# Kernel tuning notes

Hardware: AMD Instinct MI355X
Metric: run time of the kernel (lower is better)

Reference implementation:

```python
import jax, jax.numpy as jnp
import numpy as np
from jax import lax

FEAT = 56  # features_size
SR = 2     # sr_ratio
NUM_HEADS = 8

# Constant relative-distance indices, shape (N, N, 2) with values in [0, 2*FEAT-2]
_idx = np.array([[i, j] for i in range(FEAT) for j in range(FEAT)])
REL = jnp.asarray(_idx[None, :, :] - _idx[:, None, :] + FEAT - 1)  # (N, N, 2)


def setup_inputs() -> dict:
    key = jax.random.key(0)
    ks = jax.random.split(key, 8)
    dim = 256
    B = 4
    x = jax.random.normal(ks[0], (B, dim, FEAT, FEAT), dtype=jnp.float32)
    Wq = jax.random.normal(ks[1], (dim, dim), dtype=jnp.float32) * 0.02
    Wkv = jax.random.normal(ks[2], (dim, 2 * dim), dtype=jnp.float32) * 0.02
    sr_w = jax.random.normal(ks[3], (dim, dim, SR, SR), dtype=jnp.float32) * 0.02  # OIHW
    sr_b = jnp.zeros((dim,), dtype=jnp.float32)
    ln_g = jnp.ones((dim,), dtype=jnp.float32)
    ln_b = jnp.zeros((dim,), dtype=jnp.float32)
    pos_emb = jax.random.normal(ks[4], (2 * FEAT - 1, 2 * FEAT - 1), dtype=jnp.float32) * 0.2
    proj_w = jax.random.normal(ks[5], (dim, dim), dtype=jnp.float32) * 0.02
    proj_b = jnp.zeros((dim,), dtype=jnp.float32)
    return {"x": x, "Wq": Wq, "Wkv": Wkv, "sr_w": sr_w, "sr_b": sr_b,
            "ln_g": ln_g, "ln_b": ln_b, "pos_emb": pos_emb,
            "proj_w": proj_w, "proj_b": proj_b}


def reference(x, Wq, Wkv, sr_w, sr_b, ln_g, ln_b, pos_emb, proj_w, proj_b):
    B, C, H, W = x.shape
    N = H * W
    h = NUM_HEADS
    hd = C // h
    scale = hd ** -0.5

    x_q = x.reshape(B, C, N).transpose(0, 2, 1)            # (B, N, C)
    q = (x_q @ Wq).reshape(B, N, h, hd).transpose(0, 2, 1, 3)  # (B, h, N, hd)

    # spatial reduction conv (kernel=stride=SR) + layernorm
    xr = lax.conv_general_dilated(x, sr_w, (SR, SR), 'VALID',
                                  dimension_numbers=('NCHW', 'OIHW', 'NCHW'))
    xr = xr + sr_b[None, :, None, None]
    Nk = (H // SR) * (W // SR)
    x_kv = xr.reshape(B, C, Nk).transpose(0, 2, 1)          # (B, Nk, C)
    mu = jnp.mean(x_kv, axis=-1, keepdims=True)
    var = jnp.var(x_kv, axis=-1, keepdims=True)
    x_kv = (x_kv - mu) * lax.rsqrt(var + 1e-5) * ln_g + ln_b

    # kv projection; einops '(dim h l)' split: head_dim slowest, l fastest
    kv = (x_kv @ Wkv).reshape(B, Nk, hd, h, 2)
    k = kv[..., 0].transpose(0, 3, 1, 2)                    # (B, h, Nk, hd)
    v = kv[..., 1].transpose(0, 3, 1, 2)                    # (B, h, Nk, hd)

    attn = jnp.einsum('bhnd,bhmd->bhnm', q, k) * scale      # (B, h, N, Nk)
    bias = pos_emb[REL[..., 0], REL[..., 1]][:, :Nk]        # (N, Nk)
    attn = jax.nn.softmax(attn + bias, axis=-1)

    out = jnp.einsum('bhnm,bhmd->bhnd', attn, v)            # (B, h, N, hd)
    out = out.transpose(0, 2, 1, 3).reshape(B, N, C)
    out = out @ proj_w + proj_b
    return out.transpose(0, 2, 1).reshape(B, C, H, W)
```

## Files before the change

### kernel.cpp

```cpp
#include <hip/hip_runtime.h>

typedef float f32x4 __attribute__((ext_vector_type(4)));
typedef short s16x8 __attribute__((ext_vector_type(8)));
typedef unsigned short u16x4 __attribute__((ext_vector_type(4)));

#define MFMA16(a,b,c) __builtin_amdgcn_mfma_f32_16x16x32_bf16(a,b,c,0,0,0)

#define NTOK 3136
#define NKV  784
#define NKVP 800
#define CD   256
#define NH   8
#define HD   32
#define PEW  111
#define SC2  (0.17677669529663687f * 1.4426950408889634f)

static __device__ __forceinline__ unsigned short f2b(float f){
  unsigned int u = __float_as_uint(f);
  return (unsigned short)((u + 0x7fffu + ((u>>16)&1u)) >> 16);
}
static __device__ __forceinline__ float b2f(unsigned short u){
  return __uint_as_float(((unsigned int)u)<<16);
}

__global__ void k_prepw(const float* __restrict__ Wq, const float* __restrict__ Wkv,
                        const float* __restrict__ pw, const float* __restrict__ srw,
                        unsigned short* __restrict__ WqT, unsigned short* __restrict__ WkvT,
                        unsigned short* __restrict__ pwT, unsigned short* __restrict__ srwb){
  int i = blockIdx.x*256 + threadIdx.x;
  if (i < 65536){ int nn=i>>8, kk=i&255; WqT[i] = f2b(Wq[kk*256+nn]); }
  else if (i < 196608){ int j=i-65536; int c2=j>>8, kk=j&255; WkvT[j] = f2b(Wkv[kk*512+c2]); }
  else if (i < 262144){ int j=i-196608; int cc=j>>8, kk=j&255; pwT[j] = f2b(pw[kk*256+cc]); }
  else { int j=i-262144; srwb[j] = f2b(srw[j]); }
}

__global__ void k_bias(const float* __restrict__ pos, unsigned short* __restrict__ bias2){
  int key = blockIdx.x*256 + threadIdx.x;
  int n = blockIdx.y;
  if (key >= NKVP) return;
  float v;
  if (key < NKV){
    int nr = (n*9363)>>19, nc = n - nr*56;
    int tt = (key*9363)>>19, mm = key - tt*56;
    v = pos[(tt-nr+55)*PEW + (mm-nc+55)] * 1.4426950408889634f;
  } else v = -30000.f;
  bias2[(size_t)n*NKVP + key] = f2b(v);
}

__global__ void k_pad(unsigned short* __restrict__ kb, unsigned short* __restrict__ vT){
  int i = blockIdx.x*256 + threadIdx.x;
  if (i < 16384){
    int bh=i>>9, r=i&511, key=784+(r>>5), d=r&31;
    kb[((size_t)bh*NKVP + key)*HD + d] = 0;
  } else {
    int j=i-16384;
    int bh=j>>9, r=j&511, d=r>>4, key=784+(r&15);
    vT[((size_t)bh*HD + d)*NKVP + key] = 0;
  }
}

__global__ __launch_bounds__(256) void k_qproj(const float* __restrict__ x,
      const unsigned short* __restrict__ WqT, unsigned short* __restrict__ qb){
  const int tid=threadIdx.x, wv=tid>>6, l=tid&63, g=l>>4, ln16=l&15;
  const int bI = blockIdx.x/49;
  const int n0 = (blockIdx.x%49)*64;
  const int m0 = n0 + (wv>>1)*32;
  const int c0 = blockIdx.y*64 + (wv&1)*32;
  const float* xb = x + (size_t)bI*CD*NTOK;
  f32x4 acc[2][2] = {};
  for (int k0=0; k0<CD; k0+=32){
    s16x8 a[2], bf[2];
#pragma unroll
    for (int mi=0; mi<2; ++mi){
      int n = m0 + mi*16 + ln16;
      const float* xp = xb + (size_t)(k0+g*8)*NTOK + n;
#pragma unroll
      for (int j=0;j<8;++j) a[mi][j] = (short)f2b(xp[(size_t)j*NTOK]);
    }
#pragma unroll
    for (int ni=0; ni<2; ++ni)
      bf[ni] = *(const s16x8*)&WqT[(size_t)(c0+ni*16+ln16)*CD + k0 + g*8];
#pragma unroll
    for (int mi=0;mi<2;++mi)
#pragma unroll
      for (int ni=0;ni<2;++ni) acc[mi][ni] = MFMA16(a[mi], bf[ni], acc[mi][ni]);
  }
#pragma unroll
  for (int mi=0;mi<2;++mi)
#pragma unroll
    for (int ni=0;ni<2;++ni){
      int c = c0 + ni*16 + ln16;
#pragma unroll
      for (int r=0;r<4;++r){
        int n = m0 + mi*16 + g*4 + r;
        qb[((size_t)bI*NTOK + n)*CD + c] = f2b(acc[mi][ni][r]);
      }
    }
}

__global__ __launch_bounds__(256) void k_conv(const float* __restrict__ x,
      const unsigned short* __restrict__ srwb, const float* __restrict__ srb,
      float* __restrict__ convo){
  const int tid=threadIdx.x, wv=tid>>6, l=tid&63, g=l>>4, ln16=l&15;
  const int m0 = blockIdx.x*64 + (wv>>1)*32;
  const int c0 = blockIdx.y*64 + (wv&1)*32;
  size_t abase[2];
#pragma unroll
  for (int mi=0;mi<2;++mi){
    int m = m0 + mi*16 + ln16;
    int bb = (m>=2352)?3:(m>=1568)?2:(m>=784)?1:0;
    int nk = m - bb*784;
    int pp = (nk*9363)>>18, qq = nk - pp*28;
    abase[mi] = (size_t)bb*CD*NTOK + (size_t)(2*pp)*56 + 2*qq;
  }
  const int off[8] = {0,1,56,57,3136,3137,3192,3193};
  f32x4 acc[2][2] = {};
  for (int k0=0; k0<1024; k0+=32){
    int cib = (k0>>2) + g*2;
    s16x8 a[2], bf[2];
#pragma unroll
    for (int mi=0;mi<2;++mi){
      const float* xp = x + abase[mi] + (size_t)cib*NTOK;
#pragma unroll
      for (int j=0;j<8;++j) a[mi][j] = (short)f2b(xp[off[j]]);
    }
#pragma unroll
    for (int ni=0;ni<2;++ni)
      bf[ni] = *(const s16x8*)&srwb[(size_t)(c0+ni*16+ln16)*1024 + k0 + g*8];
#pragma unroll
    for (int mi=0;mi<2;++mi)
#pragma unroll
      for (int ni=0;ni<2;++ni) acc[mi][ni] = MFMA16(a[mi], bf[ni], acc[mi][ni]);
  }
#pragma unroll
  for (int mi=0;mi<2;++mi)
#pragma unroll
    for (int ni=0;ni<2;++ni){
      int c = c0 + ni*16 + ln16;
      float bias = srb[c];
#pragma unroll
      for (int r=0;r<4;++r){
        int m = m0 + mi*16 + g*4 + r;
        convo[(size_t)m*CD + c] = acc[mi][ni][r] + bias;
      }
    }
}

__global__ void k_ln(const float* __restrict__ co, const float* __restrict__ gam,
                     const float* __restrict__ bet, unsigned short* __restrict__ kvbf){
  const int row = blockIdx.x, t = threadIdx.x;
  float v = co[(size_t)row*CD + t];
  float s = v, s2 = v*v;
#pragma unroll
  for (int o=32; o>0; o>>=1){ s += __shfl_down(s,o); s2 += __shfl_down(s2,o); }
  __shared__ float ps[4], ps2[4];
  int wid = t>>6, lane = t&63;
  if (lane==0){ ps[wid]=s; ps2[wid]=s2; }
  __syncthreads();
  if (t==0){
    float a = ps[0]+ps[1]+ps[2]+ps[3];
    float a2 = ps2[0]+ps2[1]+ps2[2]+ps2[3];
    float mu = a*(1.f/CD);
    float var = a2*(1.f/CD) - mu*mu;
    ps[0] = mu; ps2[0] = rsqrtf(var + 1e-5f);
  }
  __syncthreads();
  float mu = ps[0], rs = ps2[0];
  kvbf[(size_t)row*CD + t] = f2b((v-mu)*rs*gam[t] + bet[t]);
}

__global__ __launch_bounds__(256) void k_kv(const unsigned short* __restrict__ kvbf,
      const unsigned short* __restrict__ WkvT, unsigned short* __restrict__ kb,
      unsigned short* __restrict__ vT){
  const int tid=threadIdx.x, wv=tid>>6, l=tid&63, g=l>>4, ln16=l&15;
  const int m0 = blockIdx.x*64 + (wv>>1)*32;
  const int c0 = blockIdx.y*64 + (wv&1)*32;
  f32x4 acc[2][2] = {};
  for (int k0=0; k0<CD; k0+=32){
    s16x8 a[2], bf[2];
#pragma unroll
    for (int mi=0;mi<2;++mi)
      a[mi] = *(const s16x8*)&kvbf[(size_t)(m0+mi*16+ln16)*CD + k0 + g*8];
#pragma unroll
    for (int ni=0;ni<2;++ni)
      bf[ni] = *(const s16x8*)&WkvT[(size_t)(c0+ni*16+ln16)*CD + k0 + g*8];
#pragma unroll
    for (int mi=0;mi<2;++mi)
#pragma unroll
      for (int ni=0;ni<2;++ni) acc[mi][ni] = MFMA16(a[mi], bf[ni], acc[mi][ni]);
  }
#pragma unroll
  for (int mi=0;mi<2;++mi)
#pragma unroll
    for (int ni=0;ni<2;++ni){
      int c2 = c0 + ni*16 + ln16;
      int d = c2>>4, hh = (c2>>1)&7;
#pragma unroll
      for (int r=0;r<4;++r){
        int m = m0 + mi*16 + g*4 + r;
        int bq = (m>=2352)?3:(m>=1568)?2:(m>=784)?1:0;
        int nk = m - bq*784;
        unsigned short val = f2b(acc[mi][ni][r]);
        if (c2&1) vT[(((size_t)bq*NH+hh)*HD + d)*NKVP + nk] = val;
        else      kb[(((size_t)bq*NH+hh)*NKVP + nk)*HD + d] = val;
      }
    }
}

__global__ __launch_bounds__(256) void k_attn(const unsigned short* __restrict__ qb,
      const unsigned short* __restrict__ kb, const unsigned short* __restrict__ vT,
      const unsigned short* __restrict__ bias2, unsigned short* __restrict__ aout){
  __shared__ unsigned short Pl[4][16][40];
  const int tid=threadIdx.x, wv=tid>>6, l=tid&63, g=l>>4, ln16=l&15;
  const int bh = blockIdx.y, b = bh>>3, h = bh&7;
  const int nw = blockIdx.x*64 + wv*16;
  const s16x8 qf = *(const s16x8*)&qb[((size_t)b*NTOK + nw + ln16)*CD + h*HD + g*8];
  const unsigned short* kbp = kb + (size_t)bh*NKVP*HD;
  const unsigned short* vbp = vT + (size_t)bh*HD*NKVP;
  const unsigned short* bp  = bias2 + (size_t)(nw + ln16)*NKVP;
  f32x4 accO0 = {}, accO1 = {};
  float S = 0.f;
  const f32x4 zf = {};
  for (int ks=0; ks<NKVP; ks+=32){
    s16x8 ka0 = *(const s16x8*)&kbp[(size_t)(ks+ln16)*HD + g*8];
    s16x8 ka1 = *(const s16x8*)&kbp[(size_t)(ks+16+ln16)*HD + g*8];
    f32x4 d0 = MFMA16(ka0, qf, zf);
    f32x4 d1 = MFMA16(ka1, qf, zf);
    u16x4 bb0 = *(const u16x4*)&bp[ks + g*4];
    u16x4 bb1 = *(const u16x4*)&bp[ks + 16 + g*4];
    float p[8];
#pragma unroll
    for (int r=0;r<4;++r){
      p[r]   = exp2f(d0[r]*SC2 + b2f(bb0[r]));
      p[4+r] = exp2f(d1[r]*SC2 + b2f(bb1[r]));
    }
    S += ((p[0]+p[1])+(p[2]+p[3])) + ((p[4]+p[5])+(p[6]+p[7]));
    unsigned int w0 = (unsigned int)f2b(p[0]) | ((unsigned int)f2b(p[1])<<16);
    unsigned int w1 = (unsigned int)f2b(p[2]) | ((unsigned int)f2b(p[3])<<16);
    unsigned int w2 = (unsigned int)f2b(p[4]) | ((unsigned int)f2b(p[5])<<16);
    unsigned int w3 = (unsigned int)f2b(p[6]) | ((unsigned int)f2b(p[7])<<16);
    *(uint2*)&Pl[wv][ln16][g*4]      = make_uint2(w0, w1);
    *(uint2*)&Pl[wv][ln16][16+g*4]   = make_uint2(w2, w3);
    s16x8 pf = *(const s16x8*)&Pl[wv][ln16][g*8];
    s16x8 v0 = *(const s16x8*)&vbp[(size_t)ln16*NKVP + ks + g*8];
    s16x8 v1 = *(const s16x8*)&vbp[(size_t)(16+ln16)*NKVP + ks + g*8];
    accO0 = MFMA16(pf, v0, accO0);
    accO1 = MFMA16(pf, v1, accO1);
  }
  S += __shfl_xor(S, 16);
  S += __shfl_xor(S, 32);
#pragma unroll
  for (int r=0;r<4;++r){
    float Sr = __shfl(S, g*4 + r);
    float inv = 1.f / Sr;
    int n = nw + g*4 + r;
    aout[((size_t)b*NTOK + n)*CD + h*HD + ln16]      = f2b(accO0[r]*inv);
    aout[((size_t)b*NTOK + n)*CD + h*HD + 16 + ln16] = f2b(accO1[r]*inv);
  }
}

__global__ __launch_bounds__(256) void k_proj(const unsigned short* __restrict__ ain,
      const unsigned short* __restrict__ pwT, const float* __restrict__ pb,
      float* __restrict__ out){
  const int tid=threadIdx.x, wv=tid>>6, l=tid&63, g=l>>4, ln16=l&15;
  const int bI = blockIdx.x/49;
  const int n0 = (blockIdx.x%49)*64;
  const int m0 = n0 + (wv>>1)*32;
  const int c0 = blockIdx.y*64 + (wv&1)*32;
  f32x4 acc[2][2] = {};
  for (int k0=0; k0<CD; k0+=32){
    s16x8 a[2], bf[2];
#pragma unroll
    for (int mi=0;mi<2;++mi)
      a[mi] = *(const s16x8*)&ain[((size_t)bI*NTOK + m0+mi*16+ln16)*CD + k0 + g*8];
#pragma unroll
    for (int ni=0;ni<2;++ni)
      bf[ni] = *(const s16x8*)&pwT[(size_t)(c0+ni*16+ln16)*CD + k0 + g*8];
#pragma unroll
    for (int mi=0;mi<2;++mi)
#pragma unroll
      for (int ni=0;ni<2;++ni) acc[mi][ni] = MFMA16(a[mi], bf[ni], acc[mi][ni]);
  }
#pragma unroll
  for (int ni=0;ni<2;++ni){
    int c = c0 + ni*16 + ln16;
    float bias = pb[c];
#pragma unroll
    for (int mi=0;mi<2;++mi){
      int n = m0 + mi*16 + g*4;
      f32x4 o = acc[mi][ni];
      o[0]+=bias; o[1]+=bias; o[2]+=bias; o[3]+=bias;
      *(f32x4*)&out[((size_t)bI*CD + c)*NTOK + n] = o;
    }
  }
}

extern "C" void kernel_launch(void* const* d_in, const int* in_sizes, int n_in,
                              void* d_out, int out_size, void* d_ws, size_t ws_size,
                              hipStream_t stream){
  const float* x   = (const float*)d_in[0];
  const float* Wq  = (const float*)d_in[1];
  const float* Wkv = (const float*)d_in[2];
  const float* srw = (const float*)d_in[3];
  const float* srb = (const float*)d_in[4];
  const float* lng = (const float*)d_in[5];
  const float* lnb = (const float*)d_in[6];
  const float* pos = (const float*)d_in[7];
  const float* pw  = (const float*)d_in[8];
  const float* pb  = (const float*)d_in[9];
  float* out = (float*)d_out;

  unsigned char* p = (unsigned char*)d_ws;
  unsigned short* WqT  = (unsigned short*)(p + 0);
  unsigned short* WkvT = (unsigned short*)(p + 131072);
  unsigned short* pwT  = (unsigned short*)(p + 393216);
  unsigned short* srwb = (unsigned short*)(p + 524288);
  unsigned short* bias2= (unsigned short*)(p + 1048576);
  unsigned short* qbuf = (unsigned short*)(p + 6066176);
  float*          convo= (float*)        (p + 12488704);
  unsigned short* kvbf = (unsigned short*)(p + 15699968);
  unsigned short* kbuf = (unsigned short*)(p + 17305600);
  unsigned short* vT   = (unsigned short*)(p + 18944000);
  unsigned short* aout = (unsigned short*)(p + 20582400);

  k_prepw<<<2048, 256, 0, stream>>>(Wq, Wkv, pw, srw, WqT, WkvT, pwT, srwb);
  k_bias <<<dim3(4,3136), 256, 0, stream>>>(pos, bias2);
  k_pad  <<<128, 256, 0, stream>>>(kbuf, vT);
  k_qproj<<<dim3(196,4), 256, 0, stream>>>(x, WqT, qbuf);
  k_conv <<<dim3(49,4),  256, 0, stream>>>(x, srwb, srb, convo);
  k_ln   <<<3136, 256, 0, stream>>>(convo, lng, lnb, kvbf);
  k_kv   <<<dim3(49,8),  256, 0, stream>>>(kvbf, WkvT, kbuf, vT);
  k_attn <<<dim3(49,32), 256, 0, stream>>>(qbuf, kbuf, vT, bias2, aout);
  k_proj <<<dim3(196,4), 256, 0, stream>>>(aout, pwT, pb, out);
}
```

Before: 227.8 us.

## Pretranspose x to bf16, permute K rows to drop LDS shuffle in attention

Adds a transpose kernel that writes x as token-major bf16, so the q projection and the conv read contiguous 16-byte vectors instead of strided fp32 gathers. The conv weights are reordered to match, and the attention scale is folded into q. In attention, K rows are permuted in k_kv so the score MFMA output lands directly in the P operand layout, which removes the LDS round-trip. The bias is stored as fp32, doubling its memory traffic, and the grid order is swapped so blocks sharing a head run together; k_proj also swaps operands, giving scattered scalar output stores.

```diff
diff --git a/kernel.cpp b/kernel.cpp
--- a/kernel.cpp
+++ b/kernel.cpp
@@ -1,8 +1,9 @@
 #include <hip/hip_runtime.h>
+#include <hip/hip_bf16.h>
 
 typedef float f32x4 __attribute__((ext_vector_type(4)));
 typedef short s16x8 __attribute__((ext_vector_type(8)));
-typedef unsigned short u16x4 __attribute__((ext_vector_type(4)));
+typedef unsigned short u16x8 __attribute__((ext_vector_type(8)));
 
 #define MFMA16(a,b,c) __builtin_amdgcn_mfma_f32_16x16x32_bf16(a,b,c,0,0,0)
 
@@ -13,28 +14,31 @@
 #define NH   8
 #define HD   32
 #define PEW  111
+#define LOG2E 1.4426950408889634f
 #define SC2  (0.17677669529663687f * 1.4426950408889634f)
 
 static __device__ __forceinline__ unsigned short f2b(float f){
   unsigned int u = __float_as_uint(f);
   return (unsigned short)((u + 0x7fffu + ((u>>16)&1u)) >> 16);
 }
-static __device__ __forceinline__ float b2f(unsigned short u){
-  return __uint_as_float(((unsigned int)u)<<16);
+static __device__ __forceinline__ unsigned short f2b_fast(float f){
+  __hip_bfloat16 h = __float2bfloat16(f);
+  return *reinterpret_cast<unsigned short*>(&h);
 }
 
 __global__ void k_prepw(const float* __restrict__ Wq, const float* __restrict__ Wkv,
                         const float* __restrict__ pw, const float* __restrict__ srw,
                         unsigned short* __restrict__ WqT, unsigned short* __restrict__ WkvT,
-                        unsigned short* __restrict__ pwT, unsigned short* __restrict__ srwb){
+                        unsigned short* __restrict__ pwT, unsigned short* __restrict__ srwb2){
   int i = blockIdx.x*256 + threadIdx.x;
   if (i < 65536){ int nn=i>>8, kk=i&255; WqT[i] = f2b(Wq[kk*256+nn]); }
   else if (i < 196608){ int j=i-65536; int c2=j>>8, kk=j&255; WkvT[j] = f2b(Wkv[kk*512+c2]); }
   else if (i < 262144){ int j=i-196608; int cc=j>>8, kk=j&255; pwT[j] = f2b(pw[kk*256+cc]); }
-  else { int j=i-262144; srwb[j] = f2b(srw[j]); }
-}
-
-__global__ void k_bias(const float* __restrict__ pos, unsigned short* __restrict__ bias2){
+  else { int j=i-262144; int o=j>>10, rem=j&1023, khw=rem>>8, ci=rem&255;
+         srwb2[j] = f2b(srw[o*1024 + ci*4 + khw]); }
+}
+
+__global__ void k_bias(const float* __restrict__ pos, float* __restrict__ bias2){
   int key = blockIdx.x*256 + threadIdx.x;
   int n = blockIdx.y;
   if (key >= NKVP) return;
@@ -42,16 +46,17 @@
   if (key < NKV){
     int nr = (n*9363)>>19, nc = n - nr*56;
     int tt = (key*9363)>>19, mm = key - tt*56;
-    v = pos[(tt-nr+55)*PEW + (mm-nc+55)] * 1.4426950408889634f;
-  } else v = -30000.f;
-  bias2[(size_t)n*NKVP + key] = f2b(v);
+    v = pos[(tt-nr+55)*PEW + (mm-nc+55)] * LOG2E;
+  } else v = -100000.f;
+  bias2[(size_t)n*NKVP + key] = v;
 }
 
 __global__ void k_pad(unsigned short* __restrict__ kb, unsigned short* __restrict__ vT){
   int i = blockIdx.x*256 + threadIdx.x;
   if (i < 16384){
-    int bh=i>>9, r=i&511, key=784+(r>>5), d=r&31;
-    kb[((size_t)bh*NKVP + key)*HD + d] = 0;
+    int bh=i>>9, r=i&511, ridx=r>>5, d=r&31;
+    int row = 776 + (ridx&7) + (ridx>>3)*16;
+    kb[((size_t)bh*NKVP + row)*HD + d] = 0;
   } else {
     int j=i-16384;
     int bh=j>>9, r=j&511, d=r>>4, key=784+(r&15);
@@ -59,26 +64,43 @@
   }
 }
 
-__global__ __launch_bounds__(256) void k_qproj(const float* __restrict__ x,
+__global__ __launch_bounds__(256) void k_xt(const float* __restrict__ x,
+                                            unsigned short* __restrict__ xbf){
+  __shared__ float tile[64][65];
+  const int t = threadIdx.x;
+  const int n0 = blockIdx.x*64, c0 = blockIdx.y*64, b = blockIdx.z;
+  const int tx = t&15, ty = t>>4;
+#pragma unroll
+  for (int j=0;j<4;++j){
+    f32x4 v = *(const f32x4*)&x[(size_t)(b*CD + c0+ty+j*16)*NTOK + n0 + tx*4];
+    tile[ty+j*16][tx*4+0]=v[0]; tile[ty+j*16][tx*4+1]=v[1];
+    tile[ty+j*16][tx*4+2]=v[2]; tile[ty+j*16][tx*4+3]=v[3];
+  }
+  __syncthreads();
+  const int nr = t>>2, ccb = (t&3)*16;
+  u16x8 o0, o1;
+#pragma unroll
+  for (int u=0;u<8;++u){ o0[u] = f2b(tile[ccb+u][nr]); o1[u] = f2b(tile[ccb+8+u][nr]); }
+  unsigned short* dst = &xbf[((size_t)b*NTOK + n0+nr)*CD + c0 + ccb];
+  *(u16x8*)dst = o0;
+  *(u16x8*)(dst+8) = o1;
+}
+
+__global__ __launch_bounds__(256) void k_qproj(const unsigned short* __restrict__ xbf,
       const unsigned short* __restrict__ WqT, unsigned short* __restrict__ qb){
   const int tid=threadIdx.x, wv=tid>>6, l=tid&63, g=l>>4, ln16=l&15;
   const int bI = blockIdx.x/49;
   const int n0 = (blockIdx.x%49)*64;
   const int m0 = n0 + (wv>>1)*32;
   const int c0 = blockIdx.y*64 + (wv&1)*32;
-  const float* xb = x + (size_t)bI*CD*NTOK;
   f32x4 acc[2][2] = {};
   for (int k0=0; k0<CD; k0+=32){
     s16x8 a[2], bf[2];
 #pragma unroll
-    for (int mi=0; mi<2; ++mi){
-      int n = m0 + mi*16 + ln16;
-      const float* xp = xb + (size_t)(k0+g*8)*NTOK + n;
-#pragma unroll
-      for (int j=0;j<8;++j) a[mi][j] = (short)f2b(xp[(size_t)j*NTOK]);
-    }
-#pragma unroll
-    for (int ni=0; ni<2; ++ni)
+    for (int mi=0;mi<2;++mi)
+      a[mi] = *(const s16x8*)&xbf[((size_t)bI*NTOK + m0+mi*16+ln16)*CD + k0 + g*8];
+#pragma unroll
+    for (int ni=0;ni<2;++ni)
       bf[ni] = *(const s16x8*)&WqT[(size_t)(c0+ni*16+ln16)*CD + k0 + g*8];
 #pragma unroll
     for (int mi=0;mi<2;++mi)
@@ -93,44 +115,46 @@
 #pragma unroll
       for (int r=0;r<4;++r){
         int n = m0 + mi*16 + g*4 + r;
-        qb[((size_t)bI*NTOK + n)*CD + c] = f2b(acc[mi][ni][r]);
+        qb[((size_t)bI*NTOK + n)*CD + c] = f2b(acc[mi][ni][r] * SC2);
       }
     }
 }
 
-__global__ __launch_bounds__(256) void k_conv(const float* __restrict__ x,
-      const unsigned short* __restrict__ srwb, const float* __restrict__ srb,
+__global__ __launch_bounds__(256) void k_conv(const unsigned short* __restrict__ xbf,
+      const unsigned short* __restrict__ srwb2, const float* __restrict__ srb,
       float* __restrict__ convo){
   const int tid=threadIdx.x, wv=tid>>6, l=tid&63, g=l>>4, ln16=l&15;
   const int m0 = blockIdx.x*64 + (wv>>1)*32;
   const int c0 = blockIdx.y*64 + (wv&1)*32;
-  size_t abase[2];
+  size_t abase[2][4];
 #pragma unroll
   for (int mi=0;mi<2;++mi){
     int m = m0 + mi*16 + ln16;
     int bb = (m>=2352)?3:(m>=1568)?2:(m>=784)?1:0;
     int nk = m - bb*784;
     int pp = (nk*9363)>>18, qq = nk - pp*28;
-    abase[mi] = (size_t)bb*CD*NTOK + (size_t)(2*pp)*56 + 2*qq;
-  }
-  const int off[8] = {0,1,56,57,3136,3137,3192,3193};
+#pragma unroll
+    for (int khw=0;khw<4;++khw){
+      int kh = khw>>1, kw = khw&1;
+      abase[mi][khw] = ((size_t)bb*NTOK + (2*pp+kh)*56 + 2*qq+kw)*CD;
+    }
+  }
   f32x4 acc[2][2] = {};
-  for (int k0=0; k0<1024; k0+=32){
-    int cib = (k0>>2) + g*2;
-    s16x8 a[2], bf[2];
-#pragma unroll
-    for (int mi=0;mi<2;++mi){
-      const float* xp = x + abase[mi] + (size_t)cib*NTOK;
-#pragma unroll
-      for (int j=0;j<8;++j) a[mi][j] = (short)f2b(xp[off[j]]);
-    }
-#pragma unroll
-    for (int ni=0;ni<2;++ni)
-      bf[ni] = *(const s16x8*)&srwb[(size_t)(c0+ni*16+ln16)*1024 + k0 + g*8];
-#pragma unroll
-    for (int mi=0;mi<2;++mi)
-#pragma unroll
-      for (int ni=0;ni<2;++ni) acc[mi][ni] = MFMA16(a[mi], bf[ni], acc[mi][ni]);
+#pragma unroll
+  for (int khw=0;khw<4;++khw){
+    for (int kc=0; kc<256; kc+=32){
+      s16x8 a[2], bf[2];
+#pragma unroll
+      for (int mi=0;mi<2;++mi)
+        a[mi] = *(const s16x8*)&xbf[abase[mi][khw] + kc + g*8];
+#pragma unroll
+      for (int ni=0;ni<2;++ni)
+        bf[ni] = *(const s16x8*)&srwb2[(size_t)(c0+ni*16+ln16)*1024 + khw*256 + kc + g*8];
+#pragma unroll
+      for (int mi=0;mi<2;++mi)
+#pragma unroll
+        for (int ni=0;ni<2;++ni) acc[mi][ni] = MFMA16(a[mi], bf[ni], acc[mi][ni]);
+    }
   }
 #pragma unroll
   for (int mi=0;mi<2;++mi)
@@ -201,51 +225,55 @@
         int bq = (m>=2352)?3:(m>=1568)?2:(m>=784)?1:0;
         int nk = m - bq*784;
         unsigned short val = f2b(acc[mi][ni][r]);
-        if (c2&1) vT[(((size_t)bq*NH+hh)*HD + d)*NKVP + nk] = val;
-        else      kb[(((size_t)bq*NH+hh)*NKVP + nk)*HD + d] = val;
+        if (c2&1){
+          vT[(((size_t)bq*NH+hh)*HD + d)*NKVP + nk] = val;
+        } else {
+          int chunk = nk & ~31, pos = nk & 31;
+          int gg = pos>>3, jj = pos&7;
+          int row = (jj<4) ? (gg*4+jj) : (16 + gg*4 + (jj-4));
+          kb[(((size_t)bq*NH+hh)*NKVP + chunk + row)*HD + d] = val;
+        }
       }
     }
 }
 
 __global__ __launch_bounds__(256) void k_attn(const unsigned short* __restrict__ qb,
       const unsigned short* __restrict__ kb, const unsigned short* __restrict__ vT,
-      const unsigned short* __restrict__ bias2, unsigned short* __restrict__ aout){
-  __shared__ unsigned short Pl[4][16][40];
-  const int tid=threadIdx.x, wv=tid>>6, l=tid&63, g=l>>4, ln16=l&15;
-  const int bh = blockIdx.y, b = bh>>3, h = bh&7;
-  const int nw = blockIdx.x*64 + wv*16;
+      const float* __restrict__ bias2, unsigned short* __restrict__ aout){
+  const int tid=threadIdx.x, wv=tid>>6, l=tid&63, g=l>>4, ln16=l&15;
+  const int bh = blockIdx.x, b = bh>>3, h = bh&7;
+  const int nw = blockIdx.y*64 + wv*16;
   const s16x8 qf = *(const s16x8*)&qb[((size_t)b*NTOK + nw + ln16)*CD + h*HD + g*8];
-  const unsigned short* kbp = kb + (size_t)bh*NKVP*HD;
-  const unsigned short* vbp = vT + (size_t)bh*HD*NKVP;
-  const unsigned short* bp  = bias2 + (size_t)(nw + ln16)*NKVP;
+  const unsigned short* kptr  = kb + (size_t)bh*NKVP*HD + ln16*HD + g*8;
+  const unsigned short* vptr0 = vT + (size_t)bh*HD*NKVP + ln16*NKVP + g*8;
+  const unsigned short* vptr1 = vptr0 + 16*NKVP;
+  const float* bp = bias2 + (size_t)(nw + ln16)*NKVP + g*8;
   f32x4 accO0 = {}, accO1 = {};
   float S = 0.f;
   const f32x4 zf = {};
-  for (int ks=0; ks<NKVP; ks+=32){
-    s16x8 ka0 = *(const s16x8*)&kbp[(size_t)(ks+ln16)*HD + g*8];
-    s16x8 ka1 = *(const s16x8*)&kbp[(size_t)(ks+16+ln16)*HD + g*8];
+#pragma unroll 5
+  for (int it=0; it<25; ++it){
+    s16x8 ka0 = *(const s16x8*)(kptr);
+    s16x8 ka1 = *(const s16x8*)(kptr + 16*HD);
     f32x4 d0 = MFMA16(ka0, qf, zf);
     f32x4 d1 = MFMA16(ka1, qf, zf);
-    u16x4 bb0 = *(const u16x4*)&bp[ks + g*4];
-    u16x4 bb1 = *(const u16x4*)&bp[ks + 16 + g*4];
+    f32x4 b0 = *(const f32x4*)(bp);
+    f32x4 b1 = *(const f32x4*)(bp + 4);
     float p[8];
 #pragma unroll
     for (int r=0;r<4;++r){
-      p[r]   = exp2f(d0[r]*SC2 + b2f(bb0[r]));
-      p[4+r] = exp2f(d1[r]*SC2 + b2f(bb1[r]));
+      p[r]   = exp2f(d0[r] + b0[r]);
+      p[4+r] = exp2f(d1[r] + b1[r]);
     }
     S += ((p[0]+p[1])+(p[2]+p[3])) + ((p[4]+p[5])+(p[6]+p[7]));
-    unsigned int w0 = (unsigned int)f2b(p[0]) | ((unsigned int)f2b(p[1])<<16);
-    unsigned int w1 = (unsigned int)f2b(p[2]) | ((unsigned int)f2b(p[3])<<16);
-    unsigned int w2 = (unsigned int)f2b(p[4]) | ((unsigned int)f2b(p[5])<<16);
-    unsigned int w3 = (unsigned int)f2b(p[6]) | ((unsigned int)f2b(p[7])<<16);
-    *(uint2*)&Pl[wv][ln16][g*4]      = make_uint2(w0, w1);
-    *(uint2*)&Pl[wv][ln16][16+g*4]   = make_uint2(w2, w3);
-    s16x8 pf = *(const s16x8*)&Pl[wv][ln16][g*8];
-    s16x8 v0 = *(const s16x8*)&vbp[(size_t)ln16*NKVP + ks + g*8];
-    s16x8 v1 = *(const s16x8*)&vbp[(size_t)(16+ln16)*NKVP + ks + g*8];
+    s16x8 pf;
+#pragma unroll
+    for (int j=0;j<8;++j) pf[j] = (short)f2b_fast(p[j]);
+    s16x8 v0 = *(const s16x8*)(vptr0);
+    s16x8 v1 = *(const s16x8*)(vptr1);
     accO0 = MFMA16(pf, v0, accO0);
     accO1 = MFMA16(pf, v1, accO1);
+    kptr += 32*HD; vptr0 += 32; vptr1 += 32; bp += 32;
   }
   S += __shfl_xor(S, 16);
   S += __shfl_xor(S, 32);
@@ -265,34 +293,34 @@
   const int tid=threadIdx.x, wv=tid>>6, l=tid&63, g=l>>4, ln16=l&15;
   const int bI = blockIdx.x/49;
   const int n0 = (blockIdx.x%49)*64;
-  const int m0 = n0 + (wv>>1)*32;
-  const int c0 = blockIdx.y*64 + (wv&1)*32;
+  const int nsub = n0 + (wv&1)*32;
+  const int c0 = blockIdx.y*64 + (wv>>1)*32;
   f32x4 acc[2][2] = {};
   for (int k0=0; k0<CD; k0+=32){
     s16x8 a[2], bf[2];
 #pragma unroll
     for (int mi=0;mi<2;++mi)
-      a[mi] = *(const s16x8*)&ain[((size_t)bI*NTOK + m0+mi*16+ln16)*CD + k0 + g*8];
+      a[mi] = *(const s16x8*)&pwT[(size_t)(c0+mi*16+ln16)*CD + k0 + g*8];
 #pragma unroll
     for (int ni=0;ni<2;++ni)
-      bf[ni] = *(const s16x8*)&pwT[(size_t)(c0+ni*16+ln16)*CD + k0 + g*8];
+      bf[ni] = *(const s16x8*)&ain[((size_t)bI*NTOK + nsub+ni*16+ln16)*CD + k0 + g*8];
 #pragma unroll
     for (int mi=0;mi<2;++mi)
 #pragma unroll
       for (int ni=0;ni<2;++ni) acc[mi][ni] = MFMA16(a[mi], bf[ni], acc[mi][ni]);
   }
 #pragma unroll
-  for (int ni=0;ni<2;++ni){
-    int c = c0 + ni*16 + ln16;
-    float bias = pb[c];
-#pragma unroll
-    for (int mi=0;mi<2;++mi){
-      int n = m0 + mi*16 + g*4;
-      f32x4 o = acc[mi][ni];
-      o[0]+=bias; o[1]+=bias; o[2]+=bias; o[3]+=bias;
-      *(f32x4*)&out[((size_t)bI*CD + c)*NTOK + n] = o;
-    }
-  }
+  for (int mi=0;mi<2;++mi)
+#pragma unroll
+    for (int r=0;r<4;++r){
+      int c = c0 + mi*16 + g*4 + r;
+      float bias = pb[c];
+#pragma unroll
+      for (int ni=0;ni<2;++ni){
+        int n = nsub + ni*16 + ln16;
+        out[((size_t)bI*CD + c)*NTOK + n] = acc[mi][ni][r] + bias;
+      }
+    }
 }
 
 extern "C" void kernel_launch(void* const* d_in, const int* in_sizes, int n_in,
@@ -311,25 +339,27 @@
   float* out = (float*)d_out;
 
   unsigned char* p = (unsigned char*)d_ws;
-  unsigned short* WqT  = (unsigned short*)(p + 0);
-  unsigned short* WkvT = (unsigned short*)(p + 131072);
-  unsigned short* pwT  = (unsigned short*)(p + 393216);
-  unsigned short* srwb = (unsigned short*)(p + 524288);
-  unsigned short* bias2= (unsigned short*)(p + 1048576);
-  unsigned short* qbuf = (unsigned short*)(p + 6066176);
-  float*          convo= (float*)        (p + 12488704);
-  unsigned short* kvbf = (unsigned short*)(p + 15699968);
-  unsigned short* kbuf = (unsigned short*)(p + 17305600);
-  unsigned short* vT   = (unsigned short*)(p + 18944000);
-  unsigned short* aout = (unsigned short*)(p + 20582400);
-
-  k_prepw<<<2048, 256, 0, stream>>>(Wq, Wkv, pw, srw, WqT, WkvT, pwT, srwb);
+  unsigned short* WqT   = (unsigned short*)(p + 0);
+  unsigned short* WkvT  = (unsigned short*)(p + 131072);
+  unsigned short* pwT   = (unsigned short*)(p + 393216);
+  unsigned short* srwb2 = (unsigned short*)(p + 524288);
+  float*          bias2 = (float*)        (p + 1048576);
+  unsigned short* xbf   = (unsigned short*)(p + 11083776);
+  unsigned short* qbuf  = (unsigned short*)(p + 17506304);
+  float*          convo = (float*)        (p + 23928832);
+  unsigned short* kvbf  = (unsigned short*)(p + 27140096);
+  unsigned short* kbuf  = (unsigned short*)(p + 28745728);
+  unsigned short* vT    = (unsigned short*)(p + 30384128);
+  unsigned short* aout  = (unsigned short*)(p + 32022528);
+
+  k_prepw<<<2048, 256, 0, stream>>>(Wq, Wkv, pw, srw, WqT, WkvT, pwT, srwb2);
   k_bias <<<dim3(4,3136), 256, 0, stream>>>(pos, bias2);
   k_pad  <<<128, 256, 0, stream>>>(kbuf, vT);
-  k_qproj<<<dim3(196,4), 256, 0, stream>>>(x, WqT, qbuf);
-  k_conv <<<dim3(49,4),  256, 0, stream>>>(x, srwb, srb, convo);
+  k_xt   <<<dim3(49,4,4), 256, 0, stream>>>(x, xbf);
+  k_qproj<<<dim3(196,4), 256, 0, stream>>>(xbf, WqT, qbuf);
+  k_conv <<<dim3(49,4),  256, 0, stream>>>(xbf, srwb2, srb, convo);
   k_ln   <<<3136, 256, 0, stream>>>(convo, lng, lnb, kvbf);
   k_kv   <<<dim3(49,8),  256, 0, stream>>>(kvbf, WkvT, kbuf, vT);
-  k_attn <<<dim3(49,32), 256, 0, stream>>>(qbuf, kbuf, vT, bias2, aout);
+  k_attn <<<dim3(32,49), 256, 0, stream>>>(qbuf, kbuf, vT, bias2, aout);
   k_proj <<<dim3(196,4), 256, 0, stream>>>(aout, pwT, pb, out);
 }
```

Result: slower. 249.8 us (+9.7%).
